# Kernel optimization log

Measured on AMD Instinct MI355X. Metric: run time of the kernel, lower is better.

## Reference

```python
import jax, jax.numpy as jnp
import numpy as np

D_MODEL = 1024
N_HEADS = 16
HEAD_DIM = D_MODEL // N_HEADS


def setup_inputs() -> dict:
    key = jax.random.key(0)
    k1, k2, k3 = jax.random.split(key, 3)
    x = jax.random.normal(k1, (2, 2048, D_MODEL), dtype=jnp.float32)
    w_qkv = jax.random.normal(k2, (3 * D_MODEL, D_MODEL), dtype=jnp.float32) * 0.02
    w_out = jax.random.normal(k3, (D_MODEL, D_MODEL), dtype=jnp.float32) * 0.02
    return {"x": x, "w_qkv": w_qkv, "w_out": w_out}


def reference(x, w_qkv, w_out):
    B, T, D = x.shape
    H, Hd = N_HEADS, HEAD_DIM
    # QKV projection: Linear stores weight as [out, in] -> '...i,oi->...o'
    qkv = jnp.einsum('bti,oi->bto', x, w_qkv)              # [B, T, 3D]
    # split (3*H, Hs) group-major, chunk into q/k/v of H heads each
    qkv = qkv.reshape(B, T, 3, H, Hd)
    q = jnp.transpose(qkv[:, :, 0], (0, 2, 1, 3))          # [B, H, T, Hd]
    k = jnp.transpose(qkv[:, :, 1], (0, 2, 1, 3))
    v = jnp.transpose(qkv[:, :, 2], (0, 2, 1, 3))
    scale = 1.0 / jnp.sqrt(jnp.asarray(Hd, dtype=x.dtype))
    scores = jnp.einsum('bhqd,bhkd->bhqk', q, k) * scale   # [B, H, T, T]
    causal = jnp.tril(jnp.ones((T, T), dtype=bool))        # [T, T]
    scores = jnp.where(causal[None, None], scores, jnp.asarray(-jnp.inf, dtype=scores.dtype))
    attn = jax.nn.softmax(scores, axis=-1)
    ctx = jnp.einsum('bhqk,bhkd->bhqd', attn, v)           # [B, H, T, Hd]
    ctx = jnp.transpose(ctx, (0, 2, 1, 3)).reshape(B, T, D)
    return jnp.einsum('bti,oi->bto', ctx, w_out)
```

## Files before the change

### kernel.cpp

```cpp
#include <hip/hip_runtime.h>


typedef short short8 __attribute__((ext_vector_type(8)));
typedef float f32x4 __attribute__((ext_vector_type(4)));
typedef float f32x16 __attribute__((ext_vector_type(16)));
typedef unsigned int u32x2 __attribute__((ext_vector_type(2)));
typedef unsigned short u16;
typedef unsigned int u32;

#define T_SEQ 2048
#define N_B 2
#define N_H 16
#define HD 64
#define DM 1024
#define TRIPLE 3072

__device__ __forceinline__ u16 f2bf(float f) {
  union { float f; unsigned u; } v;
  v.f = f;
  unsigned r = v.u + 0x7fffu + ((v.u >> 16) & 1u);
  return (u16)(r >> 16);
}

__device__ __forceinline__ float bf2f(u16 x) {
  return __uint_as_float((u32)x << 16);
}

__device__ __forceinline__ u32 cvtpk(float a, float b) {
  u32 r;
  asm("v_cvt_pk_bf16_f32 %0, %1, %2" : "=v"(r) : "v"(a), "v"(b));
  return r;
}

__device__ __forceinline__ void pl32swap(u32& a, u32& b) {
  u32x2 r = __builtin_amdgcn_permlane32_swap(a, b, false, false);
  a = r[0];
  b = r[1];
}

typedef const __attribute__((address_space(1))) void gvoid;
typedef __attribute__((address_space(3))) void lvoid;

__device__ __forceinline__ void g2l16(const void* g, void* l) {
  __builtin_amdgcn_global_load_lds((gvoid*)g, (lvoid*)l, 16, 0, 0);
}

__device__ __forceinline__ void storeC(float* p, float v) { *p = v; }
__device__ __forceinline__ void storeC(u16* p, float v) { *p = f2bf(v); }

__global__ __launch_bounds__(256) void cast_all(const float4* __restrict__ x,
                                                const float4* __restrict__ wq,
                                                const float4* __restrict__ wo,
                                                ushort4* __restrict__ out) {
  int i = blockIdx.x * 256 + threadIdx.x;
  const float4* src;
  int off;
  if (i < 1048576) { src = x; off = 0; }
  else if (i < 1835008) { src = wq; off = 1048576; }
  else { src = wo; off = 1835008; }
  float4 v = src[i - off];
  ushort4 o;
  o.x = f2bf(v.x); o.y = f2bf(v.y); o.z = f2bf(v.z); o.w = f2bf(v.w);
  out[i] = o;
}

__global__ __launch_bounds__(256) void vtrans(const u16* __restrict__ qkv,
                                              u16* __restrict__ vT) {
  const int tid = threadIdx.x;
  const int w = tid >> 6, lane = tid & 63;
  const int ti = lane >> 3, di = lane & 7;
  const int h = blockIdx.y, b = blockIdx.z;
  const int t0 = blockIdx.x * 256 + w * 64 + ti * 8;

  const u16* src = qkv + (size_t)(b * T_SEQ + t0) * TRIPLE + 2 * DM + h * HD + di * 8;
  u32 x[8][4];
#pragma unroll
  for (int e = 0; e < 8; ++e) {
    union { short8 v; u32 u[4]; } cv;
    cv.v = *(const short8*)(src + (size_t)e * TRIPLE);
#pragma unroll
    for (int j = 0; j < 4; ++j) x[e][j] = cv.u[j];
  }
  u32 y[8][4];
#pragma unroll
  for (int a = 0; a < 4; ++a)
#pragma unroll
    for (int j = 0; j < 4; ++j) {
      u32 lo = x[2 * a][j], hi = x[2 * a + 1][j];
      y[2 * a][j] = (lo & 0x0000FFFFu) | (hi << 16);
      y[2 * a + 1][j] = (lo >> 16) | (hi & 0xFFFF0000u);
    }
  u16* dst = vT + ((size_t)(b * N_H + h) * HD + di * 8) * T_SEQ + t0;
#pragma unroll
  for (int dd = 0; dd < 8; ++dd) {
    union { short8 v; u32 u[4]; } cv;
#pragma unroll
    for (int a = 0; a < 4; ++a) cv.u[a] = y[2 * a + (dd & 1)][dd >> 1];
    *(short8*)(dst + (size_t)dd * T_SEQ) = cv.v;
  }
}

template <typename OutT>
__global__ __launch_bounds__(256) void gemm_bt(const u16* __restrict__ A,
                                               const u16* __restrict__ W,
                                               OutT* __restrict__ C,
                                               int M, int N, int K) {
  __shared__ char As[128 * 64 * 2];
  __shared__ char Bs[128 * 64 * 2];
  const int tid = threadIdx.x;
  const int lane = tid & 63, w = tid >> 6;
  const int l15 = lane & 15, l4 = lane >> 4;
  const int m0 = blockIdx.y * 128, n0 = blockIdx.x * 128;
  const int wr = (w >> 1) * 64, wc = (w & 1) * 64;

  const f32x4 zero = {0.f, 0.f, 0.f, 0.f};
  f32x4 acc[4][4];
#pragma unroll
  for (int m = 0; m < 4; ++m)
#pragma unroll
    for (int n = 0; n < 4; ++n) acc[m][n] = zero;

  for (int k0 = 0; k0 < K; k0 += 64) {
#pragma unroll
    for (int i = 0; i < 4; ++i) {
      const int cb = (i * 4 + w) * 64;
      const int c = cb + lane;
      const int row = c >> 3;
      const int ks = ((c & 7) ^ (row & 7)) * 8;
      g2l16(A + (size_t)(m0 + row) * K + k0 + ks, As + (size_t)cb * 16);
      g2l16(W + (size_t)(n0 + row) * K + k0 + ks, Bs + (size_t)cb * 16);
    }
    __syncthreads();

#pragma unroll
    for (int kk = 0; kk < 2; ++kk) {
      short8 a[4], b[4];
#pragma unroll
      for (int m = 0; m < 4; ++m) {
        int row = wr + m * 16 + l15;
        int slot = (kk * 4 + l4) ^ (row & 7);
        a[m] = *(const short8*)(As + row * 128 + slot * 16);
      }
#pragma unroll
      for (int n = 0; n < 4; ++n) {
        int row = wc + n * 16 + l15;
        int slot = (kk * 4 + l4) ^ (row & 7);
        b[n] = *(const short8*)(Bs + row * 128 + slot * 16);
      }
#pragma unroll
      for (int m = 0; m < 4; ++m)
#pragma unroll
        for (int n = 0; n < 4; ++n)
          acc[m][n] = __builtin_amdgcn_mfma_f32_16x16x32_bf16(a[m], b[n], acc[m][n], 0, 0, 0);
    }
    __syncthreads();
  }

#pragma unroll
  for (int m = 0; m < 4; ++m)
#pragma unroll
    for (int n = 0; n < 4; ++n)
#pragma unroll
      for (int r = 0; r < 4; ++r) {
        int row = m0 + wr + m * 16 + l4 * 4 + r;
        int col = n0 + wc + n * 16 + l15;
        storeC(C + (size_t)row * N + col, acc[m][n][r]);
      }
}

__global__ __launch_bounds__(128) void attn_fwd(const u16* __restrict__ qkv,
                                                const u16* __restrict__ vT,
                                                u16* __restrict__ ctx) {
  __shared__ char Ks[3][8192];
  __shared__ char Vs[3][8192];

  const int tid = threadIdx.x;
  const int lane = tid & 63, w = tid >> 6;
  const int l31 = lane & 31, hi = lane >> 5;
  const int g = blockIdx.x;
  const int p = blockIdx.y;
  const int h = g & 15, b = g >> 4;
  const int q0A = 64 * p, q0B = 64 * (31 - p);

  const float c_log2 = 0.18033688011112042f;
  short8 qa2[2][4];
#pragma unroll
  for (int ps = 0; ps < 2; ++ps) {
    const int qq0 = ps ? q0B : q0A;
    const u16* qp = qkv + (size_t)(b * T_SEQ + qq0 + w * 32 + l31) * TRIPLE + h * HD + hi * 8;
#pragma unroll
    for (int kst = 0; kst < 4; ++kst) {
      short8 raw = *(const short8*)(qp + kst * 16);
      union { short8 v; u32 w4[4]; } qq;
#pragma unroll
      for (int j = 0; j < 4; ++j)
        qq.w4[j] = cvtpk(bf2f((u16)raw[2 * j]) * c_log2,
                         bf2f((u16)raw[2 * j + 1]) * c_log2);
      qa2[ps][kst] = qq.v;
    }
  }

  const int r0 = tid >> 3, c0 = tid & 7;
  const int swz = (c0 ^ (r0 & 7)) << 3;
  const u16* kbase = qkv + (size_t)(b * T_SEQ + r0) * TRIPLE + DM + h * HD + swz;
  const u16* vbase = vT + ((size_t)g * HD + r0) * T_SEQ + swz;

#define STAGE(kt_, buf_)                                                        \
  {                                                                             \
    _Pragma("unroll") for (int i_ = 0; i_ < 4; ++i_) {                          \
      g2l16(kbase + (size_t)((kt_) * 64 + 16 * i_) * TRIPLE,                    \
            Ks[buf_] + tid * 16 + 2048 * i_);                                   \
      g2l16(vbase + (size_t)(16 * i_) * T_SEQ + (kt_) * 64,                     \
            Vs[buf_] + tid * 16 + 2048 * i_);                                   \
    }                                                                           \
  }

  const f32x16 zero16 = {0,0,0,0,0,0,0,0,0,0,0,0,0,0,0,0};
  f32x16 o[2];
  o[0] = zero16; o[1] = zero16;
  float mr = -INFINITY, lr = 0.f;
  short8 qa_0 = qa2[0][0], qa_1 = qa2[0][1], qa_2 = qa2[0][2], qa_3 = qa2[0][3];
  int q0 = q0A;

  STAGE(0, 0);
  {
    const int kt1 = (1 <= p) ? 1 : 31;
    STAGE(kt1, 1);
  }
  asm volatile("s_waitcnt vmcnt(8)\n\ts_barrier" ::: "memory");

  int cur = 0;
  for (int i = 0;; ++i) {
    const int kt = (i <= p) ? i : 32 - i;

    if (i + 2 <= 32) {
      const int nkt2 = (i + 2 <= p) ? i + 2 : 30 - i;
      int sb = cur - 1;
      if (sb < 0) sb = 2;
      STAGE(nkt2, sb);
    }

    f32x16 s[2];
    s[0] = zero16; s[1] = zero16;
    __builtin_amdgcn_s_setprio(1);
#pragma unroll
    for (int kst = 0; kst < 4; ++kst) {
      const short8 qa = (kst == 0) ? qa_0 : (kst == 1) ? qa_1 : (kst == 2) ? qa_2 : qa_3;
      const int slot = ((kst * 2 + hi) ^ (l31 & 7)) << 4;
      short8 k0f = *(const short8*)(Ks[cur] + l31 * 128 + slot);
      s[0] = __builtin_amdgcn_mfma_f32_32x32x16_bf16(k0f, qa, s[0], 0, 0, 0);
      short8 k1f = *(const short8*)(Ks[cur] + (32 + l31) * 128 + slot);
      s[1] = __builtin_amdgcn_mfma_f32_32x32x16_bf16(k1f, qa, s[1], 0, 0, 0);
    }
    __builtin_amdgcn_s_setprio(0);

    if (i == p || i == p + 1) {
      const int qrow = q0 + w * 32 + l31;
      const int kb0 = kt * 64 + 4 * hi;
#pragma unroll
      for (int r = 0; r < 16; ++r) {
        const int key = kb0 + (r & 3) + 8 * (r >> 2);
        if (key > qrow) s[0][r] = -INFINITY;
        if (key + 32 > qrow) s[1][r] = -INFINITY;
      }
    }

    float tA = fmaxf(s[0][0], s[1][0]);
    float tB = fmaxf(s[0][1], s[1][1]);
    float tC = fmaxf(s[0][2], s[1][2]);
    float tD = fmaxf(s[0][3], s[1][3]);
#pragma unroll
    for (int r = 4; r < 16; r += 4) {
      tA = fmaxf(tA, fmaxf(s[0][r], s[1][r]));
      tB = fmaxf(tB, fmaxf(s[0][r + 1], s[1][r + 1]));
      tC = fmaxf(tC, fmaxf(s[0][r + 2], s[1][r + 2]));
      tD = fmaxf(tD, fmaxf(s[0][r + 3], s[1][r + 3]));
    }
    float mx = fmaxf(fmaxf(tA, tB), fmaxf(tC, tD));
    mx = fmaxf(mx, __shfl_xor(mx, 32));
    if (!__all(mx - mr <= 8.0f)) {
      const float mn = fmaxf(mr, mx);
      const float fr = exp2f(mr - mn);
      lr *= fr;
#pragma unroll
      for (int r = 0; r < 16; ++r) { o[0][r] *= fr; o[1][r] *= fr; }
      mr = mn;
    }
    {
      float pA = 0.f, pB = 0.f, pC = 0.f, pD = 0.f;
#pragma unroll
      for (int r = 0; r < 16; r += 4) {
        s[0][r] = exp2f(s[0][r] - mr); pA += s[0][r];
        s[0][r + 1] = exp2f(s[0][r + 1] - mr); pB += s[0][r + 1];
        s[0][r + 2] = exp2f(s[0][r + 2] - mr); pC += s[0][r + 2];
        s[0][r + 3] = exp2f(s[0][r + 3] - mr); pD += s[0][r + 3];
        s[1][r] = exp2f(s[1][r] - mr); pA += s[1][r];
        s[1][r + 1] = exp2f(s[1][r + 1] - mr); pB += s[1][r + 1];
        s[1][r + 2] = exp2f(s[1][r + 2] - mr); pC += s[1][r + 2];
        s[1][r + 3] = exp2f(s[1][r + 3] - mr); pD += s[1][r + 3];
      }
      lr += (pA + pB) + (pC + pD);
    }

    __builtin_amdgcn_s_setprio(1);
#pragma unroll
    for (int kf = 0; kf < 2; ++kf) {
#pragma unroll
      for (int sub = 0; sub < 2; ++sub) {
        const int base = 8 * sub;
        u32 w00 = cvtpk(s[kf][base + 0], s[kf][base + 1]);
        u32 w01 = cvtpk(s[kf][base + 2], s[kf][base + 3]);
        u32 w10 = cvtpk(s[kf][base + 4], s[kf][base + 5]);
        u32 w11 = cvtpk(s[kf][base + 6], s[kf][base + 7]);
        pl32swap(w00, w10);
        pl32swap(w01, w11);
        union { u32 u[4]; short8 v; } pw;
        pw.u[0] = w00; pw.u[1] = w01; pw.u[2] = w10; pw.u[3] = w11;
        const int ks = kf * 2 + sub;
        const int vslot = (((ks * 2 + hi) ^ (l31 & 7)) << 4);
        short8 v0 = *(const short8*)(Vs[cur] + l31 * 128 + vslot);
        o[0] = __builtin_amdgcn_mfma_f32_32x32x16_bf16(v0, pw.v, o[0], 0, 0, 0);
        short8 v1 = *(const short8*)(Vs[cur] + (32 + l31) * 128 + vslot);
        o[1] = __builtin_amdgcn_mfma_f32_32x32x16_bf16(v1, pw.v, o[1], 0, 0, 0);
      }
    }
    __builtin_amdgcn_s_setprio(0);

    if (i == p || i == 32) {
      const float lf = lr + __shfl_xor(lr, 32);
      const float inv = __builtin_amdgcn_rcpf(lf);
      u16* crow = ctx + (size_t)(b * T_SEQ + q0 + w * 32 + l31) * DM + h * HD;
#pragma unroll
      for (int df = 0; df < 2; ++df)
#pragma unroll
        for (int r = 0; r < 16; r += 2) {
          const int d = df * 32 + (r & 3) + 8 * (r >> 2) + 4 * hi;
          u32 pk = cvtpk(o[df][r] * inv, o[df][r + 1] * inv);
          *(u32*)(crow + d) = pk;
        }
      if (i == 32) break;
      o[0] = zero16; o[1] = zero16;
      mr = -INFINITY; lr = 0.f;
      qa_0 = qa2[1][0]; qa_1 = qa2[1][1]; qa_2 = qa2[1][2]; qa_3 = qa2[1][3];
      q0 = q0B;
    }

    if (i == 31)
      asm volatile("s_waitcnt vmcnt(0)\n\ts_barrier" ::: "memory");
    else
      asm volatile("s_waitcnt vmcnt(8)\n\ts_barrier" ::: "memory");
    cur = (cur == 2) ? 0 : cur + 1;
  }
#undef STAGE
}

extern "C" void kernel_launch(void* const* d_in, const int* in_sizes, int n_in,
                              void* d_out, int out_size, void* d_ws, size_t ws_size,
                              hipStream_t stream) {
  const float* x = (const float*)d_in[0];
  const float* wqkv = (const float*)d_in[1];
  const float* wout = (const float*)d_in[2];
  float* out = (float*)d_out;
  char* ws = (char*)d_ws;

  u16* xb    = (u16*)(ws);
  u16* wqkvb = (u16*)(ws + 8u * 1024 * 1024);
  u16* woutb = (u16*)(ws + 14u * 1024 * 1024);
  u16* qkvb  = (u16*)(ws + 16u * 1024 * 1024);
  u16* ctxb  = (u16*)(ws + 40u * 1024 * 1024);
  u16* vTb   = (u16*)(ws + 48u * 1024 * 1024);

  cast_all<<<8192, 256, 0, stream>>>((const float4*)x, (const float4*)wqkv,
                                     (const float4*)wout, (ushort4*)xb);

  gemm_bt<u16><<<dim3(24, 32), 256, 0, stream>>>(xb, wqkvb, qkvb, 4096, 3072, 1024);

  vtrans<<<dim3(8, N_H, N_B), 256, 0, stream>>>(qkvb, vTb);

  attn_fwd<<<dim3(32, 16), 128, 0, stream>>>(qkvb, vTb, ctxb);

  gemm_bt<float><<<dim3(8, 32), 256, 0, stream>>>(ctxb, woutb, out, 4096, 1024, 1024);
}
```

Baseline: 146.8 us.

## Split attention into single-wave 32-row query bands with 32-key tiles

Restructures the attention kernel so each block is one wave handling a 32-row query band. It iterates over 32-key tiles with a double-buffered LDS pipeline instead of the paired-band, two-wave, triple-buffered scheme. The grid grows to 2048 blocks, launched longest band first, to improve load balance and occupancy through smaller per-block LDS and no block barriers. In exchange there is no K/V sharing between waves, so global-to-LDS traffic per query roughly doubles, and there is less MFMA work per K/V fetch.

```diff
diff --git a/kernel.cpp b/kernel.cpp
--- a/kernel.cpp
+++ b/kernel.cpp
@@ -168,26 +168,24 @@
       }
 }
 
-__global__ __launch_bounds__(128) void attn_fwd(const u16* __restrict__ qkv,
-                                                const u16* __restrict__ vT,
-                                                u16* __restrict__ ctx) {
-  __shared__ char Ks[3][8192];
-  __shared__ char Vs[3][8192];
-
-  const int tid = threadIdx.x;
-  const int lane = tid & 63, w = tid >> 6;
+__global__ __launch_bounds__(64) void attn_fwd(const u16* __restrict__ qkv,
+                                               const u16* __restrict__ vT,
+                                               u16* __restrict__ ctx) {
+  __shared__ char Ks[2][4096];
+  __shared__ char Vs[2][4096];
+
+  const int lane = threadIdx.x;
   const int l31 = lane & 31, hi = lane >> 5;
   const int g = blockIdx.x;
-  const int p = blockIdx.y;
+  const int band = 63 - blockIdx.y;
   const int h = g & 15, b = g >> 4;
-  const int q0A = 64 * p, q0B = 64 * (31 - p);
+  const int q0 = 32 * band;
+  const int qrow = q0 + l31;
 
   const float c_log2 = 0.18033688011112042f;
-  short8 qa2[2][4];
-#pragma unroll
-  for (int ps = 0; ps < 2; ++ps) {
-    const int qq0 = ps ? q0B : q0A;
-    const u16* qp = qkv + (size_t)(b * T_SEQ + qq0 + w * 32 + l31) * TRIPLE + h * HD + hi * 8;
+  short8 qa[4];
+  {
+    const u16* qp = qkv + (size_t)(b * T_SEQ + qrow) * TRIPLE + h * HD + hi * 8;
 #pragma unroll
     for (int kst = 0; kst < 4; ++kst) {
       short8 raw = *(const short8*)(qp + kst * 16);
@@ -196,22 +194,24 @@
       for (int j = 0; j < 4; ++j)
         qq.w4[j] = cvtpk(bf2f((u16)raw[2 * j]) * c_log2,
                          bf2f((u16)raw[2 * j + 1]) * c_log2);
-      qa2[ps][kst] = qq.v;
-    }
-  }
-
-  const int r0 = tid >> 3, c0 = tid & 7;
-  const int swz = (c0 ^ (r0 & 7)) << 3;
-  const u16* kbase = qkv + (size_t)(b * T_SEQ + r0) * TRIPLE + DM + h * HD + swz;
-  const u16* vbase = vT + ((size_t)g * HD + r0) * T_SEQ + swz;
+      qa[kst] = qq.v;
+    }
+  }
+
+  const int kr0 = lane >> 3;
+  const int swzk = ((lane & 7) ^ kr0) << 3;
+  const u16* kbase = qkv + (size_t)(b * T_SEQ + kr0) * TRIPLE + DM + h * HD + swzk;
+  const int vd0 = lane >> 2;
+  const int swzv = ((lane & 3) ^ (vd0 & 3)) << 3;
+  const u16* vbase = vT + ((size_t)g * HD + vd0) * T_SEQ + swzv;
 
 #define STAGE(kt_, buf_)                                                        \
   {                                                                             \
     _Pragma("unroll") for (int i_ = 0; i_ < 4; ++i_) {                          \
-      g2l16(kbase + (size_t)((kt_) * 64 + 16 * i_) * TRIPLE,                    \
-            Ks[buf_] + tid * 16 + 2048 * i_);                                   \
-      g2l16(vbase + (size_t)(16 * i_) * T_SEQ + (kt_) * 64,                     \
-            Vs[buf_] + tid * 16 + 2048 * i_);                                   \
+      g2l16(kbase + (size_t)((kt_) * 32 + 8 * i_) * TRIPLE,                     \
+            Ks[buf_] + lane * 16 + 1024 * i_);                                  \
+      g2l16(vbase + (size_t)(16 * i_) * T_SEQ + (kt_) * 32,                     \
+            Vs[buf_] + lane * 16 + 1024 * i_);                                  \
     }                                                                           \
   }
 
@@ -219,62 +219,45 @@
   f32x16 o[2];
   o[0] = zero16; o[1] = zero16;
   float mr = -INFINITY, lr = 0.f;
-  short8 qa_0 = qa2[0][0], qa_1 = qa2[0][1], qa_2 = qa2[0][2], qa_3 = qa2[0][3];
-  int q0 = q0A;
 
   STAGE(0, 0);
-  {
-    const int kt1 = (1 <= p) ? 1 : 31;
-    STAGE(kt1, 1);
-  }
-  asm volatile("s_waitcnt vmcnt(8)\n\ts_barrier" ::: "memory");
-
-  int cur = 0;
-  for (int i = 0;; ++i) {
-    const int kt = (i <= p) ? i : 32 - i;
-
-    if (i + 2 <= 32) {
-      const int nkt2 = (i + 2 <= p) ? i + 2 : 30 - i;
-      int sb = cur - 1;
-      if (sb < 0) sb = 2;
-      STAGE(nkt2, sb);
-    }
-
-    f32x16 s[2];
-    s[0] = zero16; s[1] = zero16;
+
+  for (int t = 0;; ++t) {
+    const int cur = t & 1;
+
+    if (t < band) {
+      STAGE(t + 1, cur ^ 1);
+      asm volatile("s_waitcnt vmcnt(8)" ::: "memory");
+    } else {
+      asm volatile("s_waitcnt vmcnt(0)" ::: "memory");
+    }
+
+    f32x16 s = zero16;
     __builtin_amdgcn_s_setprio(1);
 #pragma unroll
     for (int kst = 0; kst < 4; ++kst) {
-      const short8 qa = (kst == 0) ? qa_0 : (kst == 1) ? qa_1 : (kst == 2) ? qa_2 : qa_3;
       const int slot = ((kst * 2 + hi) ^ (l31 & 7)) << 4;
-      short8 k0f = *(const short8*)(Ks[cur] + l31 * 128 + slot);
-      s[0] = __builtin_amdgcn_mfma_f32_32x32x16_bf16(k0f, qa, s[0], 0, 0, 0);
-      short8 k1f = *(const short8*)(Ks[cur] + (32 + l31) * 128 + slot);
-      s[1] = __builtin_amdgcn_mfma_f32_32x32x16_bf16(k1f, qa, s[1], 0, 0, 0);
+      short8 kf = *(const short8*)(Ks[cur] + l31 * 128 + slot);
+      s = __builtin_amdgcn_mfma_f32_32x32x16_bf16(kf, qa[kst], s, 0, 0, 0);
     }
     __builtin_amdgcn_s_setprio(0);
 
-    if (i == p || i == p + 1) {
-      const int qrow = q0 + w * 32 + l31;
-      const int kb0 = kt * 64 + 4 * hi;
+    if (t == band) {
+      const int kb0 = t * 32 + 4 * hi;
 #pragma unroll
       for (int r = 0; r < 16; ++r) {
         const int key = kb0 + (r & 3) + 8 * (r >> 2);
-        if (key > qrow) s[0][r] = -INFINITY;
-        if (key + 32 > qrow) s[1][r] = -INFINITY;
-      }
-    }
-
-    float tA = fmaxf(s[0][0], s[1][0]);
-    float tB = fmaxf(s[0][1], s[1][1]);
-    float tC = fmaxf(s[0][2], s[1][2]);
-    float tD = fmaxf(s[0][3], s[1][3]);
+        if (key > qrow) s[r] = -INFINITY;
+      }
+    }
+
+    float tA = s[0], tB = s[1], tC = s[2], tD = s[3];
 #pragma unroll
     for (int r = 4; r < 16; r += 4) {
-      tA = fmaxf(tA, fmaxf(s[0][r], s[1][r]));
-      tB = fmaxf(tB, fmaxf(s[0][r + 1], s[1][r + 1]));
-      tC = fmaxf(tC, fmaxf(s[0][r + 2], s[1][r + 2]));
-      tD = fmaxf(tD, fmaxf(s[0][r + 3], s[1][r + 3]));
+      tA = fmaxf(tA, s[r]);
+      tB = fmaxf(tB, s[r + 1]);
+      tC = fmaxf(tC, s[r + 2]);
+      tD = fmaxf(tD, s[r + 3]);
     }
     float mx = fmaxf(fmaxf(tA, tB), fmaxf(tC, tD));
     mx = fmaxf(mx, __shfl_xor(mx, 32));
@@ -290,67 +273,48 @@
       float pA = 0.f, pB = 0.f, pC = 0.f, pD = 0.f;
 #pragma unroll
       for (int r = 0; r < 16; r += 4) {
-        s[0][r] = exp2f(s[0][r] - mr); pA += s[0][r];
-        s[0][r + 1] = exp2f(s[0][r + 1] - mr); pB += s[0][r + 1];
-        s[0][r + 2] = exp2f(s[0][r + 2] - mr); pC += s[0][r + 2];
-        s[0][r + 3] = exp2f(s[0][r + 3] - mr); pD += s[0][r + 3];
-        s[1][r] = exp2f(s[1][r] - mr); pA += s[1][r];
-        s[1][r + 1] = exp2f(s[1][r + 1] - mr); pB += s[1][r + 1];
-        s[1][r + 2] = exp2f(s[1][r + 2] - mr); pC += s[1][r + 2];
-        s[1][r + 3] = exp2f(s[1][r + 3] - mr); pD += s[1][r + 3];
+        s[r] = exp2f(s[r] - mr); pA += s[r];
+        s[r + 1] = exp2f(s[r + 1] - mr); pB += s[r + 1];
+        s[r + 2] = exp2f(s[r + 2] - mr); pC += s[r + 2];
+        s[r + 3] = exp2f(s[r + 3] - mr); pD += s[r + 3];
       }
       lr += (pA + pB) + (pC + pD);
     }
 
     __builtin_amdgcn_s_setprio(1);
 #pragma unroll
-    for (int kf = 0; kf < 2; ++kf) {
-#pragma unroll
-      for (int sub = 0; sub < 2; ++sub) {
-        const int base = 8 * sub;
-        u32 w00 = cvtpk(s[kf][base + 0], s[kf][base + 1]);
-        u32 w01 = cvtpk(s[kf][base + 2], s[kf][base + 3]);
-        u32 w10 = cvtpk(s[kf][base + 4], s[kf][base + 5]);
-        u32 w11 = cvtpk(s[kf][base + 6], s[kf][base + 7]);
-        pl32swap(w00, w10);
-        pl32swap(w01, w11);
-        union { u32 u[4]; short8 v; } pw;
-        pw.u[0] = w00; pw.u[1] = w01; pw.u[2] = w10; pw.u[3] = w11;
-        const int ks = kf * 2 + sub;
-        const int vslot = (((ks * 2 + hi) ^ (l31 & 7)) << 4);
-        short8 v0 = *(const short8*)(Vs[cur] + l31 * 128 + vslot);
-        o[0] = __builtin_amdgcn_mfma_f32_32x32x16_bf16(v0, pw.v, o[0], 0, 0, 0);
-        short8 v1 = *(const short8*)(Vs[cur] + (32 + l31) * 128 + vslot);
-        o[1] = __builtin_amdgcn_mfma_f32_32x32x16_bf16(v1, pw.v, o[1], 0, 0, 0);
-      }
+    for (int sub = 0; sub < 2; ++sub) {
+      const int base = 8 * sub;
+      u32 w00 = cvtpk(s[base + 0], s[base + 1]);
+      u32 w01 = cvtpk(s[base + 2], s[base + 3]);
+      u32 w10 = cvtpk(s[base + 4], s[base + 5]);
+      u32 w11 = cvtpk(s[base + 6], s[base + 7]);
+      pl32swap(w00, w10);
+      pl32swap(w01, w11);
+      union { u32 u[4]; short8 v; } pw;
+      pw.u[0] = w00; pw.u[1] = w01; pw.u[2] = w10; pw.u[3] = w11;
+      const int vslot = ((sub * 2 + hi) ^ (l31 & 3)) << 4;
+      short8 v0 = *(const short8*)(Vs[cur] + l31 * 64 + vslot);
+      o[0] = __builtin_amdgcn_mfma_f32_32x32x16_bf16(v0, pw.v, o[0], 0, 0, 0);
+      short8 v1 = *(const short8*)(Vs[cur] + (32 + l31) * 64 + vslot);
+      o[1] = __builtin_amdgcn_mfma_f32_32x32x16_bf16(v1, pw.v, o[1], 0, 0, 0);
     }
     __builtin_amdgcn_s_setprio(0);
 
-    if (i == p || i == 32) {
-      const float lf = lr + __shfl_xor(lr, 32);
-      const float inv = __builtin_amdgcn_rcpf(lf);
-      u16* crow = ctx + (size_t)(b * T_SEQ + q0 + w * 32 + l31) * DM + h * HD;
-#pragma unroll
-      for (int df = 0; df < 2; ++df)
-#pragma unroll
-        for (int r = 0; r < 16; r += 2) {
-          const int d = df * 32 + (r & 3) + 8 * (r >> 2) + 4 * hi;
-          u32 pk = cvtpk(o[df][r] * inv, o[df][r + 1] * inv);
-          *(u32*)(crow + d) = pk;
-        }
-      if (i == 32) break;
-      o[0] = zero16; o[1] = zero16;
-      mr = -INFINITY; lr = 0.f;
-      qa_0 = qa2[1][0]; qa_1 = qa2[1][1]; qa_2 = qa2[1][2]; qa_3 = qa2[1][3];
-      q0 = q0B;
-    }
-
-    if (i == 31)
-      asm volatile("s_waitcnt vmcnt(0)\n\ts_barrier" ::: "memory");
-    else
-      asm volatile("s_waitcnt vmcnt(8)\n\ts_barrier" ::: "memory");
-    cur = (cur == 2) ? 0 : cur + 1;
-  }
+    if (t == band) break;
+  }
+
+  lr += __shfl_xor(lr, 32);
+  const float inv = __builtin_amdgcn_rcpf(lr);
+  u16* crow = ctx + (size_t)(b * T_SEQ + qrow) * DM + h * HD;
+#pragma unroll
+  for (int df = 0; df < 2; ++df)
+#pragma unroll
+    for (int r = 0; r < 16; r += 2) {
+      const int d = df * 32 + (r & 3) + 8 * (r >> 2) + 4 * hi;
+      u32 pk = cvtpk(o[df][r] * inv, o[df][r + 1] * inv);
+      *(u32*)(crow + d) = pk;
+    }
 #undef STAGE
 }
 
@@ -377,7 +341,7 @@
 
   vtrans<<<dim3(8, N_H, N_B), 256, 0, stream>>>(qkvb, vTb);
 
-  attn_fwd<<<dim3(32, 16), 128, 0, stream>>>(qkvb, vTb, ctxb);
+  attn_fwd<<<dim3(32, 64), 64, 0, stream>>>(qkvb, vTb, ctxb);
 
   gemm_bt<float><<<dim3(8, 32), 256, 0, stream>>>(ctxb, woutb, out, 4096, 1024, 1024);
 }
```

Result: slower. 151.4 us (+3.2%).
